# Kernel tuning notes

Measured on AMD Instinct MI355X. Metric: run time of the kernel, lower is better.

## Reference

```python
import jax, jax.numpy as jnp
import numpy as np

NEG_SLOPE = 0.2  # PyG GATv2Conv default negative_slope


def _gatv2_layer(x, src, dst, Wl, Wr, att, bias, heads, out_ch, concat, num_nodes):
    # x: [N, F_in]; src/dst: [E'] (self-loops already appended)
    N, H, C = num_nodes, heads, out_ch
    xl = (x @ Wl).reshape(N, H, C)  # source-side transform (lin_l)
    xr = (x @ Wr).reshape(N, H, C)  # target-side transform (lin_r)
    m = xl[src] + xr[dst]                       # [E', H, C]
    e = jax.nn.leaky_relu(m, NEG_SLOPE)
    logits = jnp.einsum('ehc,hc->eh', e, att)   # [E', H]
    # numerically stable segment softmax over incoming edges of each dst node
    mx = jax.ops.segment_max(logits, dst, num_segments=N)   # [N, H]
    ex = jnp.exp(logits - mx[dst])
    den = jax.ops.segment_sum(ex, dst, num_segments=N)      # [N, H]
    alpha = ex / den[dst]                                    # [E', H]
    out = jax.ops.segment_sum(alpha[:, :, None] * xl[src], dst, num_segments=N)  # [N, H, C]
    out = out.reshape(N, H * C) if concat else out.mean(axis=1)
    return out + bias


def setup_inputs() -> dict:
    key = jax.random.key(0)
    N, E = 50000, 800000
    IN, HID, OUT, HEADS = 128, 32, 64, 4
    ks = jax.random.split(key, 16)
    x = jax.random.normal(ks[0], (N, IN), dtype=jnp.float32)
    edge_index = jax.random.randint(ks[1], (2, E), 0, N, dtype=jnp.int64)

    def lin(k, fin, fout):
        return jax.random.normal(k, (fin, fout), dtype=jnp.float32) * (1.0 / np.sqrt(fin))

    HC = HID * HEADS  # 128
    inp = {
        'x': x, 'edge_index': edge_index,
        # layer 1: IN -> HID x HEADS, concat
        'Wl1': lin(ks[2], IN, HC), 'Wr1': lin(ks[3], IN, HC),
        'a1': jax.random.normal(ks[4], (HEADS, HID), dtype=jnp.float32) * 0.1,
        'b1': jnp.zeros((HC,), dtype=jnp.float32),
        # layer 2: HC -> HID x HEADS, concat
        'Wl2': lin(ks[5], HC, HC), 'Wr2': lin(ks[6], HC, HC),
        'a2': jax.random.normal(ks[7], (HEADS, HID), dtype=jnp.float32) * 0.1,
        'b2': jnp.zeros((HC,), dtype=jnp.float32),
        # layer 3: HC -> OUT, heads=1, concat=False
        'Wl3': lin(ks[8], HC, OUT), 'Wr3': lin(ks[9], HC, OUT),
        'a3': jax.random.normal(ks[10], (1, OUT), dtype=jnp.float32) * 0.1,
        'b3': jnp.zeros((OUT,), dtype=jnp.float32),
    }
    return inp


def reference(x, edge_index, Wl1, Wr1, a1, b1, Wl2, Wr2, a2, b2, Wl3, Wr3, a3, b3):
    N = x.shape[0]
    # PyG GATv2Conv default add_self_loops=True
    loops = jnp.arange(N, dtype=edge_index.dtype)
    src = jnp.concatenate([edge_index[0], loops])
    dst = jnp.concatenate([edge_index[1], loops])
    HID, HEADS, OUT = 32, 4, 64
    h = _gatv2_layer(x, src, dst, Wl1, Wr1, a1, b1, HEADS, HID, True, N)
    h = jax.nn.elu(h)  # eval mode: dropout is identity
    h = _gatv2_layer(h, src, dst, Wl2, Wr2, a2, b2, HEADS, HID, True, N)
    h = jax.nn.elu(h)
    out = _gatv2_layer(h, src, dst, Wl3, Wr3, a3, b3, 1, OUT, False, N)
    return out
```

## Files before the change

kernel.cpp:

```cpp
#include <hip/hip_runtime.h>
#include <cstdint>
#include <cstddef>
#include <math.h>

#define NEG_SLOPE 0.2f
#define DEGB 512
#define EB 4096

typedef unsigned short ushort_t;
typedef __attribute__((ext_vector_type(8))) short short8;
typedef __attribute__((ext_vector_type(4))) float f32x4;
typedef _Float16 half8 __attribute__((ext_vector_type(8)));
typedef _Float16 half2_t __attribute__((ext_vector_type(2)));

__device__ __forceinline__ ushort_t f2bf(float f) {
    unsigned u = __float_as_uint(f);
    unsigned r = u + 0x7FFFu + ((u >> 16) & 1u);
    return (ushort_t)(r >> 16);
}
__device__ __forceinline__ float bf2f(ushort_t h) {
    return __uint_as_float(((unsigned)h) << 16);
}
__device__ __forceinline__ ushort_t f2h(float f) {
    _Float16 h = (_Float16)f;
    return *(ushort_t*)&h;
}

__device__ __forceinline__ float dot2acc(half2_t a, half2_t b, float c) {
#if __has_builtin(__builtin_amdgcn_fdot2)
    return __builtin_amdgcn_fdot2(a, b, c, false);
#else
    return c + (float)a[0] * (float)b[0] + (float)a[1] * (float)b[1];
#endif
}

template<int CTRL>
__device__ __forceinline__ float dpp_add(float p) {
    int t = __builtin_amdgcn_update_dpp(0, __builtin_bit_cast(int, p),
                                        CTRL, 0xF, 0xF, true);
    return p + __builtin_bit_cast(float, t);
}

__device__ __forceinline__ float swz4_add(float p) {
    int t = __builtin_amdgcn_ds_swizzle(__builtin_bit_cast(int, p), 0x101F);
    return p + __builtin_bit_cast(float, t);
}

__device__ __forceinline__ int wave_incl_scan(int v, int lane) {
    #pragma unroll
    for (int o = 1; o < 64; o <<= 1) {
        int t = __shfl_up(v, o, 64);
        if (lane >= o) v += t;
    }
    return v;
}


__global__ void bucket_hist(const int* __restrict__ ei, int E, int Et,
                            int* __restrict__ blkcnt) {
    __shared__ int cnt[256];
    int t = threadIdx.x;
    cnt[t] = 0;
    __syncthreads();
    int e0 = blockIdx.x * EB;
    #pragma unroll
    for (int it = 0; it < EB / 256; ++it) {
        int e = e0 + it * 256 + t;
        if (e < Et) {
            int d = (e < E) ? ei[E + e] : (e - E);
            atomicAdd(&cnt[d >> 8], 1);
        }
    }
    __syncthreads();
    blkcnt[blockIdx.x * 256 + t] = cnt[t];
}

__global__ void colscan(int* __restrict__ blkcnt, int nblk, int* __restrict__ btot) {
    int b = blockIdx.x;
    int lane = threadIdx.x;
    int running = 0;
    for (int base = 0; base < nblk; base += 64) {
        int idx = base + lane;
        int v = (idx < nblk) ? blkcnt[idx * 256 + b] : 0;
        int incl = wave_incl_scan(v, lane);
        if (idx < nblk) blkcnt[idx * 256 + b] = running + incl - v;
        running += __shfl(incl, 63, 64);
    }
    if (lane == 0) btot[b] = running;
}

__global__ void bucketscan(const int* __restrict__ btot, int* __restrict__ bbase) {
    __shared__ int tmp[256];
    int t = threadIdx.x;
    int v = btot[t];
    tmp[t] = v;
    __syncthreads();
    for (int o = 1; o < 256; o <<= 1) {
        int x = (t >= o) ? tmp[t - o] : 0;
        __syncthreads();
        tmp[t] += x;
        __syncthreads();
    }
    bbase[t] = tmp[t] - v;
}

__global__ void bucket_scatter(const int* __restrict__ ei, int E, int Et,
                               const int* __restrict__ blkrel,
                               const int* __restrict__ bbase,
                               unsigned* __restrict__ ebuf) {
    __shared__ int base_l[256];
    __shared__ int cnt[256];
    int t = threadIdx.x;
    base_l[t] = bbase[t] + blkrel[blockIdx.x * 256 + t];
    cnt[t] = 0;
    __syncthreads();
    int e0 = blockIdx.x * EB;
    #pragma unroll
    for (int it = 0; it < EB / 256; ++it) {
        int e = e0 + it * 256 + t;
        if (e < Et) {
            int s, d;
            if (e < E) { s = ei[e]; d = ei[E + e]; }
            else       { s = d = e - E; }
            int b = d >> 8;
            int r = atomicAdd(&cnt[b], 1);
            ebuf[base_l[b] + r] = (unsigned)s | (((unsigned)d & 255u) << 17);
        }
    }
}

__global__ void csr_count(const unsigned* __restrict__ ebuf,
                          const int* __restrict__ bbase,
                          const int* __restrict__ btot,
                          int N, int* __restrict__ deg) {
    __shared__ int dcnt[256];
    int b = blockIdx.x, t = threadIdx.x;
    dcnt[t] = 0;
    __syncthreads();
    int s0 = bbase[b], c = btot[b];
    for (int i = t; i < c; i += 256)
        atomicAdd(&dcnt[ebuf[s0 + i] >> 17], 1);
    __syncthreads();
    int node = b * 256 + t;
    if (node < N) deg[node] = dcnt[t];
}

__global__ void csr_scatter2(const unsigned* __restrict__ ebuf,
                             const int* __restrict__ bbase,
                             const int* __restrict__ btot,
                             const int* __restrict__ rowstart,
                             int N, int* __restrict__ csr_src) {
    __shared__ int cur[256];
    int b = blockIdx.x, t = threadIdx.x;
    int node = b * 256 + t;
    cur[t] = (node < N) ? rowstart[node] : 0;
    __syncthreads();
    int s0 = bbase[b], c = btot[b];
    for (int i = t; i < c; i += 256) {
        unsigned v = ebuf[s0 + i];
        int pos = atomicAdd(&cur[v >> 17], 1);
        csr_src[pos] = (int)(v & 0x1FFFFu);
    }
}

__global__ void scan1(const int* __restrict__ deg, int N,
                      int* __restrict__ excl, int* __restrict__ partials) {
    __shared__ int tmp[256];
    int i = blockIdx.x * 256 + threadIdx.x;
    int v = (i < N) ? deg[i] : 0;
    tmp[threadIdx.x] = v;
    __syncthreads();
    for (int o = 1; o < 256; o <<= 1) {
        int t = (threadIdx.x >= (unsigned)o) ? tmp[threadIdx.x - o] : 0;
        __syncthreads();
        tmp[threadIdx.x] += t;
        __syncthreads();
    }
    if (i < N) excl[i] = tmp[threadIdx.x] - v;
    if (threadIdx.x == 255) partials[blockIdx.x] = tmp[255];
}

__global__ void scan23(int* __restrict__ excl, const int* __restrict__ partials,
                       int nb, int N, int* __restrict__ cursor) {
    __shared__ int tmp[256];
    int t = threadIdx.x;
    tmp[t] = (t < nb) ? partials[t] : 0;
    __syncthreads();
    for (int o = 1; o < 256; o <<= 1) {
        int x = (t >= o) ? tmp[t - o] : 0;
        __syncthreads();
        tmp[t] += x;
        __syncthreads();
    }
    int off = (blockIdx.x > 0) ? tmp[blockIdx.x - 1] : 0;
    int i = blockIdx.x * 256 + t;
    if (i < N) {
        int v = excl[i] + off;
        excl[i] = v;
        cursor[i] = v;
    }
}

__global__ void deg_hist_blk(const int* __restrict__ deg, int N,
                             int* __restrict__ dhist) {
    __shared__ int h[DEGB];
    int t = threadIdx.x;
    for (int b = t; b < DEGB; b += 256) h[b] = 0;
    __syncthreads();
    int i = blockIdx.x * 256 + t;
    if (i < N) {
        int d = deg[i]; if (d > DEGB - 1) d = DEGB - 1;
        atomicAdd(&h[d], 1);
    }
    __syncthreads();
    for (int b = t; b < DEGB; b += 256) {
        int c = h[b];
        if (c) atomicAdd(&dhist[b], c);
    }
}
__global__ void deg_scan(const int* __restrict__ dhist, int* __restrict__ dstart) {
    __shared__ int tmp[DEGB];
    int t = threadIdx.x;
    tmp[t] = dhist[t];
    __syncthreads();
    for (int o = 1; o < DEGB; o <<= 1) {
        int v = (t >= o) ? tmp[t - o] : 0;
        __syncthreads();
        tmp[t] += v;
        __syncthreads();
    }
    int total = tmp[DEGB - 1];
    dstart[t] = total - tmp[t];
}
__global__ void deg_scatter_blk(const int* __restrict__ deg,
                                const int* __restrict__ rowstart, int N,
                                int* __restrict__ dstart, int4* __restrict__ desc) {
    __shared__ int h[DEGB];
    __shared__ int base[DEGB];
    int t = threadIdx.x;
    for (int b = t; b < DEGB; b += 256) h[b] = 0;
    __syncthreads();
    int i = blockIdx.x * 256 + t;
    int dv = 0, dc = 0, r = 0;
    if (i < N) {
        dv = deg[i];
        dc = dv < DEGB - 1 ? dv : DEGB - 1;
        r = atomicAdd(&h[dc], 1);
    }
    __syncthreads();
    for (int b = t; b < DEGB; b += 256) {
        int c = h[b];
        if (c) base[b] = atomicAdd(&dstart[b], c);
    }
    __syncthreads();
    if (i < N) desc[base[dc] + r] = make_int4(i, rowstart[i], dv, 0);
}

template<int MOUT, bool CONVA>
__global__ __launch_bounds__(256) void gemm_mfma(const ushort_t* __restrict__ Ah,
                                                 const ushort_t* __restrict__ Al,
                                                 const float* __restrict__ Af,
                                                 const float* __restrict__ Wl,
                                                 const float* __restrict__ Wr,
                                                 ushort_t* __restrict__ xlh,
                                                 ushort_t* __restrict__ xrh, int N) {
    __shared__ __align__(16) ushort_t Bh[8192];
    __shared__ __align__(16) ushort_t Bl[8192];
    const int tid   = threadIdx.x;
    const int row0  = blockIdx.x * 128;
    const int col0v = blockIdx.y * 64;
    const bool isR  = col0v >= MOUT;
    const float* W  = isR ? Wr : Wl;
    const int wcol0 = isR ? (col0v - MOUT) : col0v;
    ushort_t* OUT   = isR ? xrh : xlh;

    #pragma unroll
    for (int i = 0; i < 8; ++i) {
        int idx = tid * 8 + i;
        int k   = idx >> 4;
        int c4  = (idx & 15) * 4;
        float4 w = *(const float4*)(W + (size_t)k * MOUT + wcol0 + c4);
        float wv[4] = {w.x, w.y, w.z, w.w};
        int q = k >> 5, quad = (k >> 3) & 3, j = k & 7;
        #pragma unroll
        for (int e = 0; e < 4; ++e) {
            int c = c4 + e;
            int t = c >> 4;
            int l = (quad << 4) | (c & 15);
            int pos = ((t * 4 + q) * 64 + l) * 8 + j;
            ushort_t hb = f2bf(wv[e]);
            Bh[pos] = hb;
            Bl[pos] = f2bf(wv[e] - bf2f(hb));
        }
    }
    __syncthreads();

    const int wv_  = tid >> 6;
    const int lane = tid & 63;
    const int m    = lane & 15;
    const int quad = lane >> 4;
    const int wrow0 = row0 + wv_ * 32;

    f32x4 acc[2][4] = {};

    for (int q = 0; q < 4; ++q) {
        short8 ahf[2], alf[2];
        #pragma unroll
        for (int r = 0; r < 2; ++r) {
            int row = wrow0 + 16 * r + m;
            row = row < N ? row : N - 1;
            size_t off = (size_t)row * 128 + q * 32 + quad * 8;
            if constexpr (CONVA) {
                float4 f0 = *(const float4*)(Af + off);
                float4 f1 = *(const float4*)(Af + off + 4);
                float fv[8] = {f0.x, f0.y, f0.z, f0.w, f1.x, f1.y, f1.z, f1.w};
                short ah[8], al[8];
                #pragma unroll
                for (int e = 0; e < 8; ++e) {
                    ushort_t hb = f2bf(fv[e]);
                    ah[e] = (short)hb;
                    al[e] = (short)f2bf(fv[e] - bf2f(hb));
                }
                ahf[r] = short8{ah[0],ah[1],ah[2],ah[3],ah[4],ah[5],ah[6],ah[7]};
                alf[r] = short8{al[0],al[1],al[2],al[3],al[4],al[5],al[6],al[7]};
            } else {
                ahf[r] = *(const short8*)(Ah + off);
                alf[r] = *(const short8*)(Al + off);
            }
        }
        #pragma unroll
        for (int t = 0; t < 4; ++t) {
            int base = ((t * 4 + q) * 64 + lane) * 8;
            short8 bh = *(const short8*)(Bh + base);
            short8 bl = *(const short8*)(Bl + base);
            #pragma unroll
            for (int r = 0; r < 2; ++r) {
                acc[r][t] = __builtin_amdgcn_mfma_f32_16x16x32_bf16(ahf[r], bh, acc[r][t], 0, 0, 0);
                acc[r][t] = __builtin_amdgcn_mfma_f32_16x16x32_bf16(ahf[r], bl, acc[r][t], 0, 0, 0);
                acc[r][t] = __builtin_amdgcn_mfma_f32_16x16x32_bf16(alf[r], bh, acc[r][t], 0, 0, 0);
            }
        }
    }

    #pragma unroll
    for (int r = 0; r < 2; ++r)
        #pragma unroll
        for (int i = 0; i < 4; ++i) {
            int row = wrow0 + 16 * r + quad * 4 + i;
            if (row < N) {
                #pragma unroll
                for (int t = 0; t < 4; ++t)
                    OUT[(size_t)row * MOUT + wcol0 + t * 16 + m] = f2h(acc[r][t][i]);
            }
        }
}

template<int H, int C, bool ELU, int OMODE>
__global__ __launch_bounds__(512) void node_attn(const ushort_t* __restrict__ xlh,
                                                 const ushort_t* __restrict__ xrh,
                                                 const float* __restrict__ att,
                                                 const float* __restrict__ bias,
                                                 const int4* __restrict__ desc,
                                                 const int* __restrict__ csr_src,
                                                 int N, float* __restrict__ out,
                                                 ushort_t* __restrict__ outh,
                                                 ushort_t* __restrict__ outl) {
    constexpr int HC  = H * C;
    constexpr int VPT = 8;
    constexpr int LPG = HC / VPT;
    constexpr int GPW = 64 / LPG;
    constexpr int GROUP = C / VPT;
    constexpr int DR  = 5;

    const int lane = threadIdx.x & 63;
    const int wv   = threadIdx.x >> 6;
    const int gid  = lane / LPG;
    const int lig  = lane % LPG;
    const int ch0  = lig * VPT;

    const int g0      = (blockIdx.x * 8 + wv) * GPW + gid;
    const int gstride = gridDim.x * 8 * GPW;

    half2_t a2[4];
    {
        float4 u0 = *(const float4*)(att + ch0);
        float4 u1 = *(const float4*)(att + ch0 + 4);
        a2[0] = half2_t{(_Float16)u0.x, (_Float16)u0.y};
        a2[1] = half2_t{(_Float16)u0.z, (_Float16)u0.w};
        a2[2] = half2_t{(_Float16)u1.x, (_Float16)u1.y};
        a2[3] = half2_t{(_Float16)u1.z, (_Float16)u1.w};
    }
    float bias8[VPT];
    {
        float4 b0 = *(const float4*)(bias + ch0);
        float4 b1 = *(const float4*)(bias + ch0 + 4);
        bias8[0]=b0.x; bias8[1]=b0.y; bias8[2]=b0.z; bias8[3]=b0.w;
        bias8[4]=b1.x; bias8[5]=b1.y; bias8[6]=b1.z; bias8[7]=b1.w;
    }
    const half2_t c02 = half2_t{(_Float16)NEG_SLOPE, (_Float16)NEG_SLOPE};

    if (g0 >= N) return;

    int4  dsc = desc[g0];
    half8 xrv = *(const half8*)(xrh + (size_t)dsc.x * HC + ch0);

    for (int s = g0; s < N; s += gstride) {
        const int n  = dsc.x;
        const int j0 = dsc.y;
        const int dg = dsc.z;

        const int s2 = s + gstride;
        const int4 dsc2 = desc[s2 < N ? s2 : s];

        auto ldidx = [&](int e) {
            int ee = e < dg ? e : dg - 1;
            return csr_src[j0 + ee];
        };
        auto ldrow = [&](int idx) -> half8 {
            return *(const half8*)(xlh + (size_t)(unsigned)idx * HC + ch0);
        };

        float d = 0.f;
        float acc[VPT] = {};

        auto process = [&](half8 v) {
            float p = 0.f;
            #pragma unroll
            for (int i = 0; i < 4; ++i) {
                half2_t v2 = half2_t{v[2 * i], v[2 * i + 1]};
                half2_t x2 = half2_t{xrv[2 * i], xrv[2 * i + 1]};
                half2_t m2 = v2 + x2;
                half2_t lr = __builtin_elementwise_max(m2, c02 * m2);
                p = dot2acc(lr, a2[i], p);
            }
            if constexpr (GROUP >= 2) p = dpp_add<0xB1>(p);
            if constexpr (GROUP >= 4) p = dpp_add<0x4E>(p);
            if constexpr (GROUP >= 8) p = swz4_add(p);
            float pe = __expf(p);
            d += pe;
            #pragma unroll
            for (int i = 0; i < VPT; ++i)
                acc[i] += pe * (float)v[i];
        };

        int   ibuf[DR];
        half8 rbuf[DR];
        #pragma unroll
        for (int k = 0; k < DR; ++k) ibuf[k] = ldidx(k);
        #pragma unroll
        for (int k = 0; k < DR; ++k) {
            rbuf[k] = ldrow(ibuf[k]);
            ibuf[k] = ldidx(k + DR);
        }

        int e = 0;
        for (; e + DR <= dg; e += DR) {
            #pragma unroll
            for (int k = 0; k < DR; ++k) {
                half8 v = rbuf[k];
                rbuf[k] = ldrow(ibuf[k]);
                ibuf[k] = ldidx(e + k + 2 * DR);
                process(v);
            }
        }
        #pragma unroll
        for (int k = 0; k < DR; ++k)
            if (e + k < dg) process(rbuf[k]);

        half8 xrv2 = *(const half8*)(xrh + (size_t)dsc2.x * HC + ch0);

        float inv = 1.f / d;
        float vv[VPT];
        #pragma unroll
        for (int i = 0; i < VPT; ++i) {
            float v = acc[i] * inv + bias8[i];
            if (ELU) v = v > 0.f ? v : (__expf(v) - 1.f);
            vv[i] = v;
        }
        if (OMODE == 0) {
            *(float4*)(out + (size_t)n * HC + ch0) =
                make_float4(vv[0], vv[1], vv[2], vv[3]);
            *(float4*)(out + (size_t)n * HC + ch0 + 4) =
                make_float4(vv[4], vv[5], vv[6], vv[7]);
        } else {
            ushort_t hb[VPT], lb[VPT];
            #pragma unroll
            for (int i = 0; i < VPT; ++i) {
                hb[i] = f2bf(vv[i]);
                lb[i] = f2bf(vv[i] - bf2f(hb[i]));
            }
            *(ushort4*)(outh + (size_t)n * HC + ch0) =
                ushort4{hb[0], hb[1], hb[2], hb[3]};
            *(ushort4*)(outh + (size_t)n * HC + ch0 + 4) =
                ushort4{hb[4], hb[5], hb[6], hb[7]};
            *(ushort4*)(outl + (size_t)n * HC + ch0) =
                ushort4{lb[0], lb[1], lb[2], lb[3]};
            *(ushort4*)(outl + (size_t)n * HC + ch0 + 4) =
                ushort4{lb[4], lb[5], lb[6], lb[7]};
        }

        dsc = dsc2;
        xrv = xrv2;
    }
}

extern "C" void kernel_launch(void* const* d_in, const int* in_sizes, int n_in,
                              void* d_out, int out_size, void* d_ws, size_t ws_size,
                              hipStream_t stream) {
    const float* x   = (const float*)d_in[0];
    const int*   ei  = (const int*)d_in[1];
    const float* Wl1 = (const float*)d_in[2];
    const float* Wr1 = (const float*)d_in[3];
    const float* a1  = (const float*)d_in[4];
    const float* b1  = (const float*)d_in[5];
    const float* Wl2 = (const float*)d_in[6];
    const float* Wr2 = (const float*)d_in[7];
    const float* a2  = (const float*)d_in[8];
    const float* b2  = (const float*)d_in[9];
    const float* Wl3 = (const float*)d_in[10];
    const float* Wr3 = (const float*)d_in[11];
    const float* a3  = (const float*)d_in[12];
    const float* b3  = (const float*)d_in[13];

    const int N  = in_sizes[0] / 128;
    const int E  = in_sizes[1] / 2;
    const int Et = E + N;
    const int nb = (N + 255) / 256;

    char* p = (char*)d_ws;
    auto alloc = [&](size_t bytes) -> void* {
        void* r = (void*)p;
        p += (bytes + 255) & ~(size_t)255;
        return r;
    };
    const int ebBlocks = (Et + EB - 1) / EB;
    int*      csr_src  = (int*)alloc((size_t)Et * 4 + 256);
    unsigned* ebuf     = (unsigned*)alloc((size_t)Et * 4);
    int*      blkcnt   = (int*)alloc((size_t)ebBlocks * 256 * 4);
    int*      btot     = (int*)alloc(256 * 4);
    int*      bbase    = (int*)alloc(256 * 4);
    int*      deg      = (int*)alloc((size_t)N * 4);
    int*      rowstart = (int*)alloc((size_t)N * 4);
    int*      cursor   = (int*)alloc((size_t)N * 4);
    int*      partials = (int*)alloc((size_t)nb * 4);
    int4*     desc     = (int4*)alloc((size_t)N * 16);
    int*      dhist    = (int*)alloc((size_t)DEGB * 4);
    int*      dstart   = (int*)alloc((size_t)DEGB * 4);
    ushort_t* xlh      = (ushort_t*)alloc((size_t)N * 128 * 2);
    ushort_t* xrh      = (ushort_t*)alloc((size_t)N * 128 * 2);
    ushort_t* Ah       = (ushort_t*)alloc((size_t)N * 128 * 2);
    ushort_t* Al       = (ushort_t*)alloc((size_t)N * 128 * 2);

    const int rowBlocks    = (N + 127) / 128;
    const int nodeBlocks12 = (N + 63) / 64;
    const int nodeBlocks3  = (N + 127) / 128;

    hipMemsetAsync(dhist, 0, (size_t)DEGB * 4, stream);
    bucket_hist<<<ebBlocks, 256, 0, stream>>>(ei, E, Et, blkcnt);
    colscan<<<256, 64, 0, stream>>>(blkcnt, ebBlocks, btot);
    bucketscan<<<1, 256, 0, stream>>>(btot, bbase);
    bucket_scatter<<<ebBlocks, 256, 0, stream>>>(ei, E, Et, blkcnt, bbase, ebuf);
    csr_count<<<nb, 256, 0, stream>>>(ebuf, bbase, btot, N, deg);
    scan1<<<nb, 256, 0, stream>>>(deg, N, rowstart, partials);
    scan23<<<nb, 256, 0, stream>>>(rowstart, partials, nb, N, cursor);
    csr_scatter2<<<nb, 256, 0, stream>>>(ebuf, bbase, btot, rowstart, N, csr_src);
    deg_hist_blk<<<nb, 256, 0, stream>>>(deg, N, dhist);
    deg_scan<<<1, DEGB, 0, stream>>>(dhist, dstart);
    deg_scatter_blk<<<nb, 256, 0, stream>>>(deg, rowstart, N, dstart, desc);

    gemm_mfma<128, true><<<dim3(rowBlocks, 4), 256, 0, stream>>>(
        nullptr, nullptr, x, Wl1, Wr1, xlh, xrh, N);
    node_attn<4, 32, true, 1><<<nodeBlocks12, 512, 0, stream>>>(
        xlh, xrh, a1, b1, desc, csr_src, N, nullptr, Ah, Al);

    gemm_mfma<128, false><<<dim3(rowBlocks, 4), 256, 0, stream>>>(
        Ah, Al, nullptr, Wl2, Wr2, xlh, xrh, N);
    node_attn<4, 32, true, 1><<<nodeBlocks12, 512, 0, stream>>>(
        xlh, xrh, a2, b2, desc, csr_src, N, nullptr, Ah, Al);

    float* out = (float*)d_out;
    gemm_mfma<64, false><<<dim3(rowBlocks, 2), 256, 0, stream>>>(
        Ah, Al, nullptr, Wl3, Wr3, xlh, xrh, N);
    node_attn<1, 64, false, 0><<<nodeBlocks3, 512, 0, stream>>>(
        xlh, xrh, a3, b3, desc, csr_src, N, out, nullptr, nullptr);
}
```

Measured before the change: 315.1 us.

## Fuse CSR build kernels and launch one node per group in attention

Merges the degree count, block scan, degree histogram, scan finalisation and CSR/descriptor scatter kernels into three kernels, cutting seven preprocessing launches to three. It also drops the grid-stride loop with next-descriptor prefetch in node_attn, so each group handles exactly one node and the grid doubles. The aim is lower launch overhead and more parallelism in the attention kernels. The cost is losing the cross-node prefetch of the next descriptor and xr row.

Measured after the change: 297.2 us. 5.7% less time.

```diff
diff --git a/kernel.cpp b/kernel.cpp
--- a/kernel.cpp
+++ b/kernel.cpp
@@ -129,31 +129,95 @@
     }
 }
 
-__global__ void csr_count(const unsigned* __restrict__ ebuf,
-                          const int* __restrict__ bbase,
-                          const int* __restrict__ btot,
-                          int N, int* __restrict__ deg) {
+__global__ void bucket_deg_scan_hist(const unsigned* __restrict__ ebuf,
+                                     const int* __restrict__ bbase,
+                                     const int* __restrict__ btot,
+                                     int N, int* __restrict__ deg,
+                                     int* __restrict__ rowstart,
+                                     int* __restrict__ partials,
+                                     int* __restrict__ dhist) {
     __shared__ int dcnt[256];
+    __shared__ int tmp[256];
+    __shared__ int h[DEGB];
     int b = blockIdx.x, t = threadIdx.x;
     dcnt[t] = 0;
+    h[t] = 0; h[t + 256] = 0;
     __syncthreads();
     int s0 = bbase[b], c = btot[b];
     for (int i = t; i < c; i += 256)
         atomicAdd(&dcnt[ebuf[s0 + i] >> 17], 1);
     __syncthreads();
     int node = b * 256 + t;
-    if (node < N) deg[node] = dcnt[t];
-}
-
-__global__ void csr_scatter2(const unsigned* __restrict__ ebuf,
-                             const int* __restrict__ bbase,
-                             const int* __restrict__ btot,
-                             const int* __restrict__ rowstart,
-                             int N, int* __restrict__ csr_src) {
+    int dv = dcnt[t];
+    if (node < N) deg[node] = dv;
+    tmp[t] = dv;
+    __syncthreads();
+    for (int o = 1; o < 256; o <<= 1) {
+        int x = (t >= o) ? tmp[t - o] : 0;
+        __syncthreads();
+        tmp[t] += x;
+        __syncthreads();
+    }
+    if (node < N) rowstart[node] = tmp[t] - dv;
+    if (t == 255) partials[b] = tmp[255];
+    if (node < N) {
+        int dc = dv < DEGB - 1 ? dv : DEGB - 1;
+        atomicAdd(&h[dc], 1);
+    }
+    __syncthreads();
+    int c0 = h[t];       if (c0) atomicAdd(&dhist[t], c0);
+    int c1 = h[t + 256]; if (c1) atomicAdd(&dhist[t + 256], c1);
+}
+
+__global__ void finalize_scans(int* __restrict__ rowstart,
+                               const int* __restrict__ partials, int nbkt, int N,
+                               const int* __restrict__ dhist,
+                               int* __restrict__ dstart) {
+    __shared__ int tmp[DEGB];
+    int t = threadIdx.x;
+    int b = blockIdx.x;
+    if (b < nbkt) {
+        if (t < 256) tmp[t] = (t < nbkt) ? partials[t] : 0;
+        __syncthreads();
+        for (int o = 1; o < 256; o <<= 1) {
+            int x = (t < 256 && t >= o) ? tmp[t - o] : 0;
+            __syncthreads();
+            if (t < 256) tmp[t] += x;
+            __syncthreads();
+        }
+        int off = (b > 0) ? tmp[b - 1] : 0;
+        int node = b * 256 + t;
+        if (t < 256 && node < N) rowstart[node] += off;
+    } else {
+        int v = dhist[t];
+        tmp[t] = v;
+        __syncthreads();
+        for (int o = 1; o < DEGB; o <<= 1) {
+            int x = (t >= o) ? tmp[t - o] : 0;
+            __syncthreads();
+            tmp[t] += x;
+            __syncthreads();
+        }
+        dstart[t] = tmp[DEGB - 1] - tmp[t];
+    }
+}
+
+__global__ void csr_perm_scatter(const unsigned* __restrict__ ebuf,
+                                 const int* __restrict__ bbase,
+                                 const int* __restrict__ btot,
+                                 const int* __restrict__ rowstart,
+                                 const int* __restrict__ deg, int N,
+                                 int* __restrict__ dstart,
+                                 int* __restrict__ csr_src,
+                                 int4* __restrict__ desc) {
     __shared__ int cur[256];
+    __shared__ int h[DEGB];
+    __shared__ int base[DEGB];
     int b = blockIdx.x, t = threadIdx.x;
     int node = b * 256 + t;
-    cur[t] = (node < N) ? rowstart[node] : 0;
+    int rs = (node < N) ? rowstart[node] : 0;
+    cur[t] = rs;
+    h[t] = 0; h[t + 256] = 0;
     __syncthreads();
     int s0 = bbase[b], c = btot[b];
     for (int i = t; i < c; i += 256) {
@@ -161,99 +225,15 @@
         int pos = atomicAdd(&cur[v >> 17], 1);
         csr_src[pos] = (int)(v & 0x1FFFFu);
     }
-}
-
-__global__ void scan1(const int* __restrict__ deg, int N,
-                      int* __restrict__ excl, int* __restrict__ partials) {
-    __shared__ int tmp[256];
-    int i = blockIdx.x * 256 + threadIdx.x;
-    int v = (i < N) ? deg[i] : 0;
-    tmp[threadIdx.x] = v;
-    __syncthreads();
-    for (int o = 1; o < 256; o <<= 1) {
-        int t = (threadIdx.x >= (unsigned)o) ? tmp[threadIdx.x - o] : 0;
-        __syncthreads();
-        tmp[threadIdx.x] += t;
-        __syncthreads();
-    }
-    if (i < N) excl[i] = tmp[threadIdx.x] - v;
-    if (threadIdx.x == 255) partials[blockIdx.x] = tmp[255];
-}
-
-__global__ void scan23(int* __restrict__ excl, const int* __restrict__ partials,
-                       int nb, int N, int* __restrict__ cursor) {
-    __shared__ int tmp[256];
-    int t = threadIdx.x;
-    tmp[t] = (t < nb) ? partials[t] : 0;
-    __syncthreads();
-    for (int o = 1; o < 256; o <<= 1) {
-        int x = (t >= o) ? tmp[t - o] : 0;
-        __syncthreads();
-        tmp[t] += x;
-        __syncthreads();
-    }
-    int off = (blockIdx.x > 0) ? tmp[blockIdx.x - 1] : 0;
-    int i = blockIdx.x * 256 + t;
-    if (i < N) {
-        int v = excl[i] + off;
-        excl[i] = v;
-        cursor[i] = v;
-    }
-}
-
-__global__ void deg_hist_blk(const int* __restrict__ deg, int N,
-                             int* __restrict__ dhist) {
-    __shared__ int h[DEGB];
-    int t = threadIdx.x;
-    for (int b = t; b < DEGB; b += 256) h[b] = 0;
-    __syncthreads();
-    int i = blockIdx.x * 256 + t;
-    if (i < N) {
-        int d = deg[i]; if (d > DEGB - 1) d = DEGB - 1;
-        atomicAdd(&h[d], 1);
-    }
-    __syncthreads();
-    for (int b = t; b < DEGB; b += 256) {
-        int c = h[b];
-        if (c) atomicAdd(&dhist[b], c);
-    }
-}
-__global__ void deg_scan(const int* __restrict__ dhist, int* __restrict__ dstart) {
-    __shared__ int tmp[DEGB];
-    int t = threadIdx.x;
-    tmp[t] = dhist[t];
-    __syncthreads();
-    for (int o = 1; o < DEGB; o <<= 1) {
-        int v = (t >= o) ? tmp[t - o] : 0;
-        __syncthreads();
-        tmp[t] += v;
-        __syncthreads();
-    }
-    int total = tmp[DEGB - 1];
-    dstart[t] = total - tmp[t];
-}
-__global__ void deg_scatter_blk(const int* __restrict__ deg,
-                                const int* __restrict__ rowstart, int N,
-                                int* __restrict__ dstart, int4* __restrict__ desc) {
-    __shared__ int h[DEGB];
-    __shared__ int base[DEGB];
-    int t = threadIdx.x;
-    for (int b = t; b < DEGB; b += 256) h[b] = 0;
-    __syncthreads();
-    int i = blockIdx.x * 256 + t;
-    int dv = 0, dc = 0, r = 0;
-    if (i < N) {
-        dv = deg[i];
-        dc = dv < DEGB - 1 ? dv : DEGB - 1;
-        r = atomicAdd(&h[dc], 1);
-    }
-    __syncthreads();
-    for (int b = t; b < DEGB; b += 256) {
-        int c = h[b];
-        if (c) base[b] = atomicAdd(&dstart[b], c);
-    }
-    __syncthreads();
-    if (i < N) desc[base[dc] + r] = make_int4(i, rowstart[i], dv, 0);
+    int dv = (node < N) ? deg[node] : 0;
+    int dc = dv < DEGB - 1 ? dv : DEGB - 1;
+    int r = 0;
+    if (node < N) r = atomicAdd(&h[dc], 1);
+    __syncthreads();
+    int c0 = h[t];       if (c0) base[t]       = atomicAdd(&dstart[t], c0);
+    int c1 = h[t + 256]; if (c1) base[t + 256] = atomicAdd(&dstart[t + 256], c1);
+    __syncthreads();
+    if (node < N) desc[base[dc] + r] = make_int4(node, rs, dv, 0);
 }
 
 template<int MOUT, bool CONVA>
@@ -378,8 +358,8 @@
     const int lig  = lane % LPG;
     const int ch0  = lig * VPT;
 
-    const int g0      = (blockIdx.x * 8 + wv) * GPW + gid;
-    const int gstride = gridDim.x * 8 * GPW;
+    const int s = (blockIdx.x * 8 + wv) * GPW + gid;
+    if (s >= N) return;
 
     half2_t a2[4];
     {
@@ -399,108 +379,96 @@
     }
     const half2_t c02 = half2_t{(_Float16)NEG_SLOPE, (_Float16)NEG_SLOPE};
 
-    if (g0 >= N) return;
-
-    int4  dsc = desc[g0];
-    half8 xrv = *(const half8*)(xrh + (size_t)dsc.x * HC + ch0);
-
-    for (int s = g0; s < N; s += gstride) {
-        const int n  = dsc.x;
-        const int j0 = dsc.y;
-        const int dg = dsc.z;
-
-        const int s2 = s + gstride;
-        const int4 dsc2 = desc[s2 < N ? s2 : s];
-
-        auto ldidx = [&](int e) {
-            int ee = e < dg ? e : dg - 1;
-            return csr_src[j0 + ee];
-        };
-        auto ldrow = [&](int idx) -> half8 {
-            return *(const half8*)(xlh + (size_t)(unsigned)idx * HC + ch0);
-        };
-
-        float d = 0.f;
-        float acc[VPT] = {};
-
-        auto process = [&](half8 v) {
-            float p = 0.f;
-            #pragma unroll
-            for (int i = 0; i < 4; ++i) {
-                half2_t v2 = half2_t{v[2 * i], v[2 * i + 1]};
-                half2_t x2 = half2_t{xrv[2 * i], xrv[2 * i + 1]};
-                half2_t m2 = v2 + x2;
-                half2_t lr = __builtin_elementwise_max(m2, c02 * m2);
-                p = dot2acc(lr, a2[i], p);
-            }
-            if constexpr (GROUP >= 2) p = dpp_add<0xB1>(p);
-            if constexpr (GROUP >= 4) p = dpp_add<0x4E>(p);
-            if constexpr (GROUP >= 8) p = swz4_add(p);
-            float pe = __expf(p);
-            d += pe;
-            #pragma unroll
-            for (int i = 0; i < VPT; ++i)
-                acc[i] += pe * (float)v[i];
-        };
-
-        int   ibuf[DR];
-        half8 rbuf[DR];
-        #pragma unroll
-        for (int k = 0; k < DR; ++k) ibuf[k] = ldidx(k);
+    const int4 dsc = desc[s];
+    const int n  = dsc.x;
+    const int j0 = dsc.y;
+    const int dg = dsc.z;
+
+    half8 xrv = *(const half8*)(xrh + (size_t)n * HC + ch0);
+
+    auto ldidx = [&](int e) {
+        int ee = e < dg ? e : dg - 1;
+        return csr_src[j0 + ee];
+    };
+    auto ldrow = [&](int idx) -> half8 {
+        return *(const half8*)(xlh + (size_t)(unsigned)idx * HC + ch0);
+    };
+
+    float d = 0.f;
+    float acc[VPT] = {};
+
+    auto process = [&](half8 v) {
+        float p = 0.f;
+        #pragma unroll
+        for (int i = 0; i < 4; ++i) {
+            half2_t v2 = half2_t{v[2 * i], v[2 * i + 1]};
+            half2_t x2 = half2_t{xrv[2 * i], xrv[2 * i + 1]};
+            half2_t m2 = v2 + x2;
+            half2_t lr = __builtin_elementwise_max(m2, c02 * m2);
+            p = dot2acc(lr, a2[i], p);
+        }
+        if constexpr (GROUP >= 2) p = dpp_add<0xB1>(p);
+        if constexpr (GROUP >= 4) p = dpp_add<0x4E>(p);
+        if constexpr (GROUP >= 8) p = swz4_add(p);
+        float pe = __expf(p);
+        d += pe;
+        #pragma unroll
+        for (int i = 0; i < VPT; ++i)
+            acc[i] += pe * (float)v[i];
+    };
+
+    int   ibuf[DR];
+    half8 rbuf[DR];
+    #pragma unroll
+    for (int k = 0; k < DR; ++k) ibuf[k] = ldidx(k);
+    #pragma unroll
+    for (int k = 0; k < DR; ++k) {
+        rbuf[k] = ldrow(ibuf[k]);
+        ibuf[k] = ldidx(k + DR);
+    }
+
+    int e = 0;
+    for (; e + DR <= dg; e += DR) {
         #pragma unroll
         for (int k = 0; k < DR; ++k) {
+            half8 v = rbuf[k];
             rbuf[k] = ldrow(ibuf[k]);
-            ibuf[k] = ldidx(k + DR);
-        }
-
-        int e = 0;
-        for (; e + DR <= dg; e += DR) {
-            #pragma unroll
-            for (int k = 0; k < DR; ++k) {
-                half8 v = rbuf[k];
-                rbuf[k] = ldrow(ibuf[k]);
-                ibuf[k] = ldidx(e + k + 2 * DR);
-                process(v);
-            }
-        }
-        #pragma unroll
-        for (int k = 0; k < DR; ++k)
-            if (e + k < dg) process(rbuf[k]);
-
-        half8 xrv2 = *(const half8*)(xrh + (size_t)dsc2.x * HC + ch0);
-
-        float inv = 1.f / d;
-        float vv[VPT];
+            ibuf[k] = ldidx(e + k + 2 * DR);
+            process(v);
+        }
+    }
+    #pragma unroll
+    for (int k = 0; k < DR; ++k)
+        if (e + k < dg) process(rbuf[k]);
+
+    float inv = 1.f / d;
+    float vv[VPT];
+    #pragma unroll
+    for (int i = 0; i < VPT; ++i) {
+        float v = acc[i] * inv + bias8[i];
+        if (ELU) v = v > 0.f ? v : (__expf(v) - 1.f);
+        vv[i] = v;
+    }
+    if (OMODE == 0) {
+        *(float4*)(out + (size_t)n * HC + ch0) =
+            make_float4(vv[0], vv[1], vv[2], vv[3]);
+        *(float4*)(out + (size_t)n * HC + ch0 + 4) =
+            make_float4(vv[4], vv[5], vv[6], vv[7]);
+    } else {
+        ushort_t hb[VPT], lb[VPT];
         #pragma unroll
         for (int i = 0; i < VPT; ++i) {
-            float v = acc[i] * inv + bias8[i];
-            if (ELU) v = v > 0.f ? v : (__expf(v) - 1.f);
-            vv[i] = v;
-        }
-        if (OMODE == 0) {
-            *(float4*)(out + (size_t)n * HC + ch0) =
-                make_float4(vv[0], vv[1], vv[2], vv[3]);
-            *(float4*)(out + (size_t)n * HC + ch0 + 4) =
-                make_float4(vv[4], vv[5], vv[6], vv[7]);
-        } else {
-            ushort_t hb[VPT], lb[VPT];
-            #pragma unroll
-            for (int i = 0; i < VPT; ++i) {
-                hb[i] = f2bf(vv[i]);
-                lb[i] = f2bf(vv[i] - bf2f(hb[i]));
-            }
-            *(ushort4*)(outh + (size_t)n * HC + ch0) =
-                ushort4{hb[0], hb[1], hb[2], hb[3]};
-            *(ushort4*)(outh + (size_t)n * HC + ch0 + 4) =
-                ushort4{hb[4], hb[5], hb[6], hb[7]};
-            *(ushort4*)(outl + (size_t)n * HC + ch0) =
-                ushort4{lb[0], lb[1], lb[2], lb[3]};
-            *(ushort4*)(outl + (size_t)n * HC + ch0 + 4) =
-                ushort4{lb[4], lb[5], lb[6], lb[7]};
-        }
-
-        dsc = dsc2;
-        xrv = xrv2;
+            hb[i] = f2bf(vv[i]);
+            lb[i] = f2bf(vv[i] - bf2f(hb[i]));
+        }
+        *(ushort4*)(outh + (size_t)n * HC + ch0) =
+            ushort4{hb[0], hb[1], hb[2], hb[3]};
+        *(ushort4*)(outh + (size_t)n * HC + ch0 + 4) =
+            ushort4{hb[4], hb[5], hb[6], hb[7]};
+        *(ushort4*)(outl + (size_t)n * HC + ch0) =
+            ushort4{lb[0], lb[1], lb[2], lb[3]};
+        *(ushort4*)(outl + (size_t)n * HC + ch0 + 4) =
+            ushort4{lb[4], lb[5], lb[6], lb[7]};
     }
 }
 
@@ -541,7 +509,6 @@
     int*      bbase    = (int*)alloc(256 * 4);
     int*      deg      = (int*)alloc((size_t)N * 4);
     int*      rowstart = (int*)alloc((size_t)N * 4);
-    int*      cursor   = (int*)alloc((size_t)N * 4);
     int*      partials = (int*)alloc((size_t)nb * 4);
     int4*     desc     = (int4*)alloc((size_t)N * 16);
     int*      dhist    = (int*)alloc((size_t)DEGB * 4);
@@ -552,21 +519,20 @@
     ushort_t* Al       = (ushort_t*)alloc((size_t)N * 128 * 2);
 
     const int rowBlocks    = (N + 127) / 128;
-    const int nodeBlocks12 = (N + 63) / 64;
-    const int nodeBlocks3  = (N + 127) / 128;
+    const int nodeBlocks12 = (N + 31) / 32;
+    const int nodeBlocks3  = (N + 63) / 64;
 
     hipMemsetAsync(dhist, 0, (size_t)DEGB * 4, stream);
     bucket_hist<<<ebBlocks, 256, 0, stream>>>(ei, E, Et, blkcnt);
     colscan<<<256, 64, 0, stream>>>(blkcnt, ebBlocks, btot);
     bucketscan<<<1, 256, 0, stream>>>(btot, bbase);
     bucket_scatter<<<ebBlocks, 256, 0, stream>>>(ei, E, Et, blkcnt, bbase, ebuf);
-    csr_count<<<nb, 256, 0, stream>>>(ebuf, bbase, btot, N, deg);
-    scan1<<<nb, 256, 0, stream>>>(deg, N, rowstart, partials);
-    scan23<<<nb, 256, 0, stream>>>(rowstart, partials, nb, N, cursor);
-    csr_scatter2<<<nb, 256, 0, stream>>>(ebuf, bbase, btot, rowstart, N, csr_src);
-    deg_hist_blk<<<nb, 256, 0, stream>>>(deg, N, dhist);
-    deg_scan<<<1, DEGB, 0, stream>>>(dhist, dstart);
-    deg_scatter_blk<<<nb, 256, 0, stream>>>(deg, rowstart, N, dstart, desc);
+    bucket_deg_scan_hist<<<nb, 256, 0, stream>>>(ebuf, bbase, btot, N,
+                                                 deg, rowstart, partials, dhist);
+    finalize_scans<<<nb + 1, DEGB, 0, stream>>>(rowstart, partials, nb, N,
+                                                dhist, dstart);
+    csr_perm_scatter<<<nb, 256, 0, stream>>>(ebuf, bbase, btot, rowstart, deg, N,
+                                             dstart, csr_src, desc);
 
     gemm_mfma<128, true><<<dim3(rowBlocks, 4), 256, 0, stream>>>(
         nullptr, nullptr, x, Wl1, Wr1, xlh, xrh, N);
```
